# Kernel tuning notes

Hardware: AMD Instinct MI355X
Metric: run time of the kernel (lower is better)

Reference implementation:

```python
import jax, jax.numpy as jnp
import numpy as np

CHUNK = 64  # chunk size for chunkwise delta-rule


def l2norm(x, eps=1e-6):
    return x * jax.lax.rsqrt(jnp.sum(x * x, axis=-1, keepdims=True) + eps)


def delta_rule_chunked(q, k, v, beta):
    """Chunkwise-parallel DeltaNet delta rule.

    Recurrence (per head): S_t = S_{t-1} + k_t u_t^T with
      u_t = beta_t * (v_t - S_{t-1}^T k_t),   o_t = S_t^T q_t.
    q,k,v: [B,H,L,D]; beta: [B,H,L]. Returns o: [B,H,L,D].
    """
    B, H, L, D = q.shape
    n = L // CHUNK
    def to_chunks(t):
        return jnp.moveaxis(t.reshape(B, H, n, CHUNK, *t.shape[4:] if t.ndim > 4 else ()) if False else t.reshape(B, H, n, CHUNK, -1) if t.ndim == 4 else t.reshape(B, H, n, CHUNK), 2, 0)
    qc = jnp.moveaxis(q.reshape(B, H, n, CHUNK, D), 2, 0)  # [n,B,H,C,D]
    kc = jnp.moveaxis(k.reshape(B, H, n, CHUNK, D), 2, 0)
    vc = jnp.moveaxis(v.reshape(B, H, n, CHUNK, D), 2, 0)
    bc = jnp.moveaxis(beta.reshape(B, H, n, CHUNK), 2, 0)   # [n,B,H,C]
    strict = jnp.tril(jnp.ones((CHUNK, CHUNK), bool), -1)
    incl = jnp.tril(jnp.ones((CHUNK, CHUNK), bool))
    eye = jnp.eye(CHUNK, dtype=q.dtype)

    def step(S, inp):
        qi, ki, vi, bi = inp  # [B,H,C,D], [B,H,C]
        kk = jnp.einsum('bhid,bhjd->bhij', ki, ki)            # [B,H,C,C]
        # Unit lower-triangular system (I + B*strict_tril(K K^T)) U = B*(V - K S)
        T = eye + jnp.where(strict, bi[..., :, None] * kk, 0.0)
        rhs = bi[..., None] * (vi - jnp.einsum('bhcd,bhde->bhce', ki, S))
        U = jax.scipy.linalg.solve_triangular(T, rhs, lower=True)
        qk = jnp.einsum('bhid,bhjd->bhij', qi, ki)
        O = jnp.einsum('bhcd,bhde->bhce', qi, S) \
            + jnp.einsum('bhij,bhje->bhie', jnp.where(incl, qk, 0.0), U)
        S_new = S + jnp.einsum('bhcd,bhce->bhde', ki, U)      # [B,H,D,D]
        return S_new, O

    S0 = jnp.zeros((B, H, D, D), q.dtype)
    _, O = jax.lax.scan(step, S0, (qc, kc, vc, bc))
    return jnp.moveaxis(O, 0, 2).reshape(B, H, L, D)


def setup_inputs() -> dict:
    key = jax.random.key(0)
    ks = jax.random.split(key, 7)
    B, C, Hh, Ww = 8, 768, 64, 64
    n_heads = 12
    s = 1.0 / np.sqrt(C)
    x = jax.random.normal(ks[0], (B, C, Hh, Ww), jnp.float32)
    Wq = jax.random.normal(ks[1], (C, C), jnp.float32) * s
    Wk = jax.random.normal(ks[2], (C, C), jnp.float32) * s
    Wv = jax.random.normal(ks[3], (C, C), jnp.float32) * s
    Wb = jax.random.normal(ks[4], (C, n_heads), jnp.float32) * s
    Wo = jax.random.normal(ks[5], (C, C), jnp.float32) * s
    return {"x": x, "Wq": Wq, "Wk": Wk, "Wv": Wv, "Wb": Wb, "Wo": Wo}


def reference(x, Wq, Wk, Wv, Wb, Wo):
    B, C, Hh, Ww = x.shape
    L = Hh * Ww
    n_heads = Wb.shape[1]
    D = C // n_heads
    t = x.reshape(B, C, L).transpose(0, 2, 1)                 # [B,L,C] tokens
    def heads(z):
        return z.reshape(B, L, n_heads, D).transpose(0, 2, 1, 3)  # [B,H,L,D]
    q = l2norm(heads(jax.nn.silu(t @ Wq)))
    k = l2norm(heads(jax.nn.silu(t @ Wk)))
    v = heads(jax.nn.silu(t @ Wv))
    beta = jax.nn.sigmoid(t @ Wb).transpose(0, 2, 1)          # [B,H,L]
    o = delta_rule_chunked(q, k, v, beta)                     # [B,H,L,D]
    o = o.transpose(0, 2, 1, 3).reshape(B, L, C)
    y = o @ Wo
    out = t + y                                               # residual
    return out.transpose(0, 2, 1).reshape(B, C, Hh, Ww)
```

## Files before the change

kernel.cpp:

```cpp
#include <hip/hip_runtime.h>


#define B_  8
#define C_  768
#define L_  4096
#define NH_ 12
#define D_  64
#define NC_ 64
#define BH_ 96

typedef unsigned short ushort_t;
typedef float f32x4 __attribute__((ext_vector_type(4)));
typedef unsigned short u16x4 __attribute__((ext_vector_type(4)));
typedef unsigned short u16x8 __attribute__((ext_vector_type(8)));
using short8 = __attribute__((ext_vector_type(8))) short;

__device__ __forceinline__ float b2f(ushort_t u) {
  union { unsigned u; float f; } x; x.u = ((unsigned)u) << 16; return x.f;
}
__device__ __forceinline__ ushort_t f2b(float f) {
  union { float f; unsigned u; } x; x.f = f;
  unsigned r = (x.u + 0x7FFFu + ((x.u >> 16) & 1u)) >> 16;
  return (ushort_t)r;
}
__device__ __forceinline__ f32x4 mfma16(short8 a, short8 b, f32x4 c) {
  return __builtin_amdgcn_mfma_f32_16x16x32_bf16(a, b, c, 0, 0, 0);
}
__device__ __forceinline__ void gload16(const ushort_t* g, ushort_t* l) {
  __builtin_amdgcn_global_load_lds(
      (const __attribute__((address_space(1))) void*)(g),
      (__attribute__((address_space(3))) void*)(l), 16, 0, 0);
}

#define SWZ(e, i) (((e) * 64) + ((i) ^ (((e) & 7) << 3)))

__global__ __launch_bounds__(256) void k_wprep(
    const float* __restrict__ W, ushort_t* __restrict__ hi,
    ushort_t* __restrict__ lo) {
  __shared__ float ts[64 * 65];
  int tid = threadIdx.x;
  int c0 = blockIdx.x * 64;
  int n0 = blockIdx.y * 64;
  #pragma unroll
  for (int it = 0; it < 4; ++it) {
    int e = tid + it * 256;
    int r = e >> 4, c4 = (e & 15) * 4;
    *(f32x4*)&ts[r * 65 + c4] =
        *(const f32x4*)(W + (size_t)(c0 + r) * C_ + n0 + c4);
  }
  __syncthreads();
  #pragma unroll
  for (int it = 0; it < 4; ++it) {
    int e = tid + it * 256;
    int n = e >> 4, r4 = (e & 15) * 4;
    u16x4 hv, lv;
    #pragma unroll
    for (int q = 0; q < 4; ++q) {
      float w = ts[(r4 + q) * 65 + n];
      ushort_t h = f2b(w);
      hv[q] = h;
      lv[q] = f2b(w - b2f(h));
    }
    *(u16x4*)(hi + (size_t)(n0 + n) * C_ + c0 + r4) = hv;
    *(u16x4*)(lo + (size_t)(n0 + n) * C_ + c0 + r4) = lv;
  }
}

__global__ __launch_bounds__(256) void k_xtr(
    const float* __restrict__ x, ushort_t* __restrict__ hi,
    ushort_t* __restrict__ lo) {
  __shared__ float ts[64 * 65];
  int tid = threadIdx.x;
  int l0 = blockIdx.x * 64;
  int c0 = blockIdx.y * 64;
  int b = blockIdx.z;
  const float* xb = x + (size_t)b * C_ * L_;
  #pragma unroll
  for (int it = 0; it < 4; ++it) {
    int e = tid + it * 256;
    int ci = e >> 4, l4 = (e & 15) * 4;
    *(f32x4*)&ts[ci * 65 + l4] =
        *(const f32x4*)(xb + (size_t)(c0 + ci) * L_ + l0 + l4);
  }
  __syncthreads();
  #pragma unroll
  for (int it = 0; it < 4; ++it) {
    int e = tid + it * 256;
    int li = e >> 4, c4 = (e & 15) * 4;
    u16x4 hv, lv;
    #pragma unroll
    for (int q = 0; q < 4; ++q) {
      float w = ts[(c4 + q) * 65 + li];
      ushort_t h = f2b(w);
      hv[q] = h;
      lv[q] = f2b(w - b2f(h));
    }
    size_t base = ((size_t)b * L_ + l0 + li) * C_ + c0 + c4;
    *(u16x4*)(hi + base) = hv;
    *(u16x4*)(lo + base) = lv;
  }
}

__global__ __launch_bounds__(256) void k_beta(
    const float* __restrict__ x, const float* __restrict__ Wb,
    float* __restrict__ beta) {
  __shared__ float wb[C_ * NH_];
  int tid = threadIdx.x;
  for (int i = tid; i < C_ * NH_; i += 256) wb[i] = Wb[i];
  __syncthreads();
  int b = blockIdx.y;
  int l = blockIdx.x * 256 + tid;
  f32x4 a0 = {0.f, 0.f, 0.f, 0.f}, a1 = a0, a2 = a0;
  const float* xb = x + (size_t)b * C_ * L_ + l;
  for (int c = 0; c < C_; ++c) {
    float xv = xb[(size_t)c * L_];
    const f32x4* wr = (const f32x4*)&wb[c * NH_];
    a0 += xv * wr[0]; a1 += xv * wr[1]; a2 += xv * wr[2];
  }
  float* bp = beta + (size_t)b * NH_ * L_ + l;
  #pragma unroll
  for (int h = 0; h < 4; ++h) {
    bp[(size_t)h * L_]       = 1.f / (1.f + expf(-a0[h]));
    bp[(size_t)(h + 4) * L_] = 1.f / (1.f + expf(-a1[h]));
    bp[(size_t)(h + 8) * L_] = 1.f / (1.f + expf(-a2[h]));
  }
}

__global__ __launch_bounds__(256) void k_qkv(
    const ushort_t* __restrict__ xhi, const ushort_t* __restrict__ xlo,
    const ushort_t* __restrict__ whi, const ushort_t* __restrict__ wlo,
    ushort_t* __restrict__ qout, ushort_t* __restrict__ kout,
    ushort_t* __restrict__ vout) {
  __shared__ __align__(16) ushort_t Ah[128 * 32];
  __shared__ __align__(16) ushort_t Al[128 * 32];
  __shared__ __align__(16) ushort_t Bh[128 * 32];
  __shared__ __align__(16) ushort_t Bl[128 * 32];
  int tid = threadIdx.x;
  int row0 = blockIdx.x * 128;
  int n0   = blockIdx.y * 128;
  int wid = tid >> 6, lane = tid & 63;
  int lr = lane & 15, lk = lane >> 4;
  f32x4 acc[2][8];
  #pragma unroll
  for (int mf = 0; mf < 2; ++mf)
    #pragma unroll
    for (int nf = 0; nf < 8; ++nf) acc[mf][nf] = (f32x4){0.f, 0.f, 0.f, 0.f};
  const ushort_t* ga  = xhi + (size_t)row0 * C_;
  const ushort_t* gal = xlo + (size_t)row0 * C_;
  const ushort_t* gb  = whi + (size_t)n0 * C_;
  const ushort_t* gbl = wlo + (size_t)n0 * C_;
  int ra0 = wid * 32 + lr, ra1 = wid * 32 + 16 + lr;
  int ua0 = ra0 * 4 + (lk ^ ((ra0 >> 1) & 3));
  int ua1 = ra1 * 4 + (lk ^ ((ra1 >> 1) & 3));
  for (int kb = 0; kb < C_; kb += 32) {
    if (kb) __syncthreads();
    #pragma unroll
    for (int c = 0; c < 2; ++c) {
      int u = tid + c * 256;
      int r = u >> 2, sp = u & 3;
      int s = sp ^ ((r >> 1) & 3);
      size_t goff = (size_t)r * C_ + kb + s * 8;
      gload16(ga  + goff, &Ah[u * 8]);
      gload16(gal + goff, &Al[u * 8]);
      gload16(gb  + goff, &Bh[u * 8]);
      gload16(gbl + goff, &Bl[u * 8]);
    }
    __syncthreads();
    short8 ah0 = *(const short8*)&Ah[ua0 * 8];
    short8 al0 = *(const short8*)&Al[ua0 * 8];
    short8 ah1 = *(const short8*)&Ah[ua1 * 8];
    short8 al1 = *(const short8*)&Al[ua1 * 8];
    #pragma unroll
    for (int nf = 0; nf < 8; ++nf) {
      int rb = nf * 16 + lr;
      int ub = rb * 4 + (lk ^ ((rb >> 1) & 3));
      short8 bh = *(const short8*)&Bh[ub * 8];
      short8 bl = *(const short8*)&Bl[ub * 8];
      acc[0][nf] = mfma16(ah0, bh, acc[0][nf]);
      acc[0][nf] = mfma16(al0, bh, acc[0][nf]);
      acc[0][nf] = mfma16(ah0, bl, acc[0][nf]);
      acc[1][nf] = mfma16(ah1, bh, acc[1][nf]);
      acc[1][nf] = mfma16(al1, bh, acc[1][nf]);
      acc[1][nf] = mfma16(ah1, bl, acc[1][nf]);
    }
  }
  #pragma unroll
  for (int mf = 0; mf < 2; ++mf)
    #pragma unroll
    for (int nf = 0; nf < 8; ++nf)
      #pragma unroll
      for (int rr = 0; rr < 4; ++rr) {
        float xv = acc[mf][nf][rr];
        acc[mf][nf][rr] = xv / (1.f + expf(-xv));
      }
  int proj = n0 / 768;
  if (proj < 2) {
    #pragma unroll
    for (int mf = 0; mf < 2; ++mf)
      #pragma unroll
      for (int rr = 0; rr < 4; ++rr)
        #pragma unroll
        for (int g = 0; g < 2; ++g) {
          float ss = 0.f;
          #pragma unroll
          for (int nf = 4 * g; nf < 4 * g + 4; ++nf)
            ss += acc[mf][nf][rr] * acc[mf][nf][rr];
          ss += __shfl_xor(ss, 1); ss += __shfl_xor(ss, 2);
          ss += __shfl_xor(ss, 4); ss += __shfl_xor(ss, 8);
          float rs = rsqrtf(ss + 1e-6f);
          #pragma unroll
          for (int nf = 4 * g; nf < 4 * g + 4; ++nf) acc[mf][nf][rr] *= rs;
        }
  }
  ushort_t* outp = (proj == 0) ? qout : ((proj == 1) ? kout : vout);
  int nc0 = n0 - proj * 768;
  #pragma unroll
  for (int mf = 0; mf < 2; ++mf) {
    int row = row0 + wid * 32 + mf * 16 + lk * 4;
    int b = row >> 12, l = row & 4095;
    #pragma unroll
    for (int nf = 0; nf < 8; ++nf) {
      int ncol = nc0 + nf * 16 + lr;
      int h = ncol >> 6, d = ncol & 63;
      ushort_t* op = outp + (((size_t)b * NH_ + h) * L_ + l) * 64 + d;
      #pragma unroll
      for (int rr = 0; rr < 4; ++rr)
        op[(size_t)rr * 64] = f2b(acc[mf][nf][rr]);
    }
  }
}

__global__ __launch_bounds__(256) void k_pre2(
    const ushort_t* __restrict__ qg, ushort_t* kg, ushort_t* vg,
    const float* __restrict__ betag, ushort_t* __restrict__ kwg,
    ushort_t* __restrict__ aqg) {
  __shared__ float As[64 * 68];
  __shared__ float XK[64 * 68];
  __shared__ float XV[64 * 68];
  int tid = threadIdx.x;
  int nc = blockIdx.x, bh = blockIdx.y;
  const size_t cb = ((size_t)bh * 64 + nc) * 4096;
  const float* bb = betag + (size_t)bh * L_ + nc * 64;
  int wid = tid >> 6, lane = tid & 63;
  int lr = lane & 15, lk = lane >> 4;
  short8 kbf[4][2], ka[2], qa[2];
  #pragma unroll
  for (int nf = 0; nf < 4; ++nf)
    #pragma unroll
    for (int ks = 0; ks < 2; ++ks)
      kbf[nf][ks] = *(const short8*)(kg + cb +
          (size_t)(nf * 16 + lr) * 64 + ks * 32 + lk * 8);
  #pragma unroll
  for (int ks = 0; ks < 2; ++ks) {
    ka[ks] = *(const short8*)(kg + cb + (size_t)(wid * 16 + lr) * 64 + ks * 32 + lk * 8);
    qa[ks] = *(const short8*)(qg + cb + (size_t)(wid * 16 + lr) * 64 + ks * 32 + lk * 8);
  }
  f32x4 kk[4], qk[4];
  #pragma unroll
  for (int nf = 0; nf < 4; ++nf) {
    kk[nf] = (f32x4){0.f, 0.f, 0.f, 0.f};
    qk[nf] = (f32x4){0.f, 0.f, 0.f, 0.f};
    kk[nf] = mfma16(ka[0], kbf[nf][0], kk[nf]);
    kk[nf] = mfma16(ka[1], kbf[nf][1], kk[nf]);
    qk[nf] = mfma16(qa[0], kbf[nf][0], qk[nf]);
    qk[nf] = mfma16(qa[1], kbf[nf][1], qk[nf]);
  }
  float bi[4];
  #pragma unroll
  for (int r = 0; r < 4; ++r) bi[r] = bb[wid * 16 + lk * 4 + r];
  #pragma unroll
  for (int r = 0; r < 4; ++r) {
    int i = wid * 16 + lk * 4 + r;
    #pragma unroll
    for (int nf = 0; nf < 4; ++nf) {
      int j = nf * 16 + lr;
      As[i * 68 + j] = (j < i) ? bi[r] * kk[nf][r] : 0.f;
      aqg[cb + (size_t)i * 64 + j] = (j <= i) ? f2b(qk[nf][r]) : (ushort_t)0;
    }
  }
  #pragma unroll
  for (int it = 0; it < 2; ++it) {
    int e = tid + it * 256;
    int i = e >> 3, c0 = (e & 7) * 8;
    float bv = bb[i];
    u16x8 kv8 = *(const u16x8*)(kg + cb + (size_t)i * 64 + c0);
    u16x8 vv8 = *(const u16x8*)(vg + cb + (size_t)i * 64 + c0);
    f32x4 klo = {bv*b2f(kv8[0]), bv*b2f(kv8[1]), bv*b2f(kv8[2]), bv*b2f(kv8[3])};
    f32x4 khi = {bv*b2f(kv8[4]), bv*b2f(kv8[5]), bv*b2f(kv8[6]), bv*b2f(kv8[7])};
    f32x4 vlo = {bv*b2f(vv8[0]), bv*b2f(vv8[1]), bv*b2f(vv8[2]), bv*b2f(vv8[3])};
    f32x4 vhi = {bv*b2f(vv8[4]), bv*b2f(vv8[5]), bv*b2f(vv8[6]), bv*b2f(vv8[7])};
    *(f32x4*)&XK[i * 68 + c0]     = klo;
    *(f32x4*)&XK[i * 68 + c0 + 4] = khi;
    *(f32x4*)&XV[i * 68 + c0]     = vlo;
    *(f32x4*)&XV[i * 68 + c0 + 4] = vhi;
  }
  __syncthreads();
  if (tid < 128) {
    float* Xc = (tid < 64) ? (XK + tid) : (XV + (tid - 64));
    float xr[32];
    #pragma unroll
    for (int i = 0; i < 32; ++i) xr[i] = Xc[i * 68];
    #pragma unroll
    for (int i = 1; i < 32; ++i) {
      float xi = xr[i];
      #pragma unroll
      for (int jb = 0; jb <= (i >> 2); ++jb) {
        f32x4 a4 = *(const f32x4*)&As[i * 68 + jb * 4];
        xi -= a4[0]*xr[jb*4] + a4[1]*xr[jb*4+1] + a4[2]*xr[jb*4+2] + a4[3]*xr[jb*4+3];
      }
      xr[i] = xi;
    }
    #pragma unroll
    for (int i = 1; i < 32; ++i) Xc[i * 68] = xr[i];
  } else {
    int ks = wid - 2;
    #pragma unroll
    for (int nf = 0; nf < 4; ++nf)
      #pragma unroll
      for (int jj = 0; jj < 8; ++jj) {
        int d = ks * 32 + lk * 8 + jj;
        kg[cb + (size_t)d * 64 + nf * 16 + lr] = (ushort_t)kbf[nf][ks][jj];
      }
  }
  __syncthreads();
  if (tid >= 128) {
    int col = tid - 128;
    float* Xc = (col < 64) ? (XK + col) : (XV + (col - 64));
    float xr[32];
    #pragma unroll
    for (int i = 0; i < 32; ++i) xr[i] = Xc[(32 + i) * 68];
    #pragma unroll
    for (int jb = 0; jb < 8; ++jb) {
      float xt0 = Xc[(jb*4+0)*68], xt1 = Xc[(jb*4+1)*68];
      float xt2 = Xc[(jb*4+2)*68], xt3 = Xc[(jb*4+3)*68];
      #pragma unroll
      for (int i = 0; i < 32; ++i) {
        f32x4 a4 = *(const f32x4*)&As[(32 + i) * 68 + jb * 4];
        xr[i] -= a4[0]*xt0 + a4[1]*xt1 + a4[2]*xt2 + a4[3]*xt3;
      }
    }
    #pragma unroll
    for (int i = 1; i < 32; ++i) {
      float xi = xr[i];
      #pragma unroll
      for (int jb = 8; jb <= ((32 + i) >> 2); ++jb) {
        f32x4 a4 = *(const f32x4*)&As[(32 + i) * 68 + jb * 4];
        xi -= a4[0]*xr[jb*4-32] + a4[1]*xr[jb*4-31]
            + a4[2]*xr[jb*4-30] + a4[3]*xr[jb*4-29];
      }
      xr[i] = xi;
    }
    #pragma unroll
    for (int i = 0; i < 32; ++i) Xc[(32 + i) * 68] = xr[i];
  } else {
    #pragma unroll
    for (int it = 0; it < 4; ++it) {
      int u = tid + it * 128;
      int i = u >> 4, d0 = (u & 15) * 4;
      f32x4 v4 = *(const f32x4*)&XK[i * 68 + d0];
      u16x4 pk = {f2b(v4[0]), f2b(v4[1]), f2b(v4[2]), f2b(v4[3])};
      *(u16x4*)(kwg + cb + (size_t)i * 64 + d0) = pk;
      f32x4 w4 = *(const f32x4*)&XV[i * 68 + d0];
      u16x4 pv = {f2b(w4[0]), f2b(w4[1]), f2b(w4[2]), f2b(w4[3])};
      *(u16x4*)(vg + cb + (size_t)i * 64 + d0) = pv;
    }
  }
  __syncthreads();
  #pragma unroll
  for (int it = 0; it < 2; ++it) {
    int u = tid + it * 256;
    int i = 32 + (u >> 4), d0 = (u & 15) * 4;
    f32x4 v4 = *(const f32x4*)&XK[i * 68 + d0];
    u16x4 pk = {f2b(v4[0]), f2b(v4[1]), f2b(v4[2]), f2b(v4[3])};
    *(u16x4*)(kwg + cb + (size_t)i * 64 + d0) = pk;
    f32x4 w4 = *(const f32x4*)&XV[i * 68 + d0];
    u16x4 pv = {f2b(w4[0]), f2b(w4[1]), f2b(w4[2]), f2b(w4[3])};
    *(u16x4*)(vg + cb + (size_t)i * 64 + d0) = pv;
  }
}

__global__ __launch_bounds__(256) void k_seq(
    const ushort_t* __restrict__ qg,  const ushort_t* __restrict__ ktg,
    const ushort_t* __restrict__ kwg, const ushort_t* __restrict__ vwg,
    const ushort_t* __restrict__ aqg, ushort_t* __restrict__ og) {
  __shared__ float    STs[64 * 64];
  __shared__ ushort_t SbT[64 * 64];
  __shared__ ushort_t UT [64 * 64];
  int tid = threadIdx.x, bh = blockIdx.x;
  int w  = tid >> 6, l = tid & 63;
  int lr = l & 15, lk = l >> 4;
  int mrow = w * 16 + lr;
  int r0   = w * 16 + lk * 4;
  for (int i = tid; i < 4096; i += 256) { STs[i] = 0.f; SbT[i] = 0; }
  int b = bh / NH_, h = bh % NH_;
  ushort_t* ob = og + (size_t)b * L_ * C_ + h * 64;
  __syncthreads();
  for (int nc = 0; nc < NC_; ++nc) {
    const size_t cb = ((size_t)bh * 64 + nc) * 4096;
    const ushort_t* Kw = kwg + cb;
    const ushort_t* Qc = qg  + cb;
    const ushort_t* Aq = aqg + cb;
    const ushort_t* KT = ktg + cb;
    const ushort_t* Vw = vwg + cb;
    short8 a_kw0 = *(const short8*)(Kw + mrow * 64 + lk * 8);
    short8 a_kw1 = *(const short8*)(Kw + mrow * 64 + 32 + lk * 8);
    short8 a_q0  = *(const short8*)(Qc + mrow * 64 + lk * 8);
    short8 a_q1  = *(const short8*)(Qc + mrow * 64 + 32 + lk * 8);
    short8 a_aq0 = *(const short8*)(Aq + mrow * 64 + lk * 8);
    short8 a_aq1 = *(const short8*)(Aq + mrow * 64 + 32 + lk * 8);
    short8 a_kt0 = *(const short8*)(KT + mrow * 64 + lk * 8);
    short8 a_kt1 = *(const short8*)(KT + mrow * 64 + 32 + lk * 8);
    float vwv[4][4];
    #pragma unroll
    for (int t = 0; t < 4; ++t)
      #pragma unroll
      for (int r = 0; r < 4; ++r)
        vwv[t][r] = b2f(Vw[(size_t)(r0 + r) * 64 + t * 16 + lr]);
    #pragma unroll
    for (int t = 0; t < 4; ++t) {
      int e = t * 16 + lr;
      f32x4 acc = {0.f, 0.f, 0.f, 0.f};
      short8 b0 = *(const short8*)(SbT + SWZ(e, lk * 8));
      short8 b1 = *(const short8*)(SbT + SWZ(e, 32 + lk * 8));
      acc = mfma16(a_kw0, b0, acc);
      acc = mfma16(a_kw1, b1, acc);
      u16x4 uo;
      #pragma unroll
      for (int r = 0; r < 4; ++r) uo[r] = f2b(vwv[t][r] - acc[r]);
      *(u16x4*)(UT + SWZ(e, r0)) = uo;
    }
    __syncthreads();
    #pragma unroll
    for (int t = 0; t < 4; ++t) {
      int e = t * 16 + lr;
      f32x4 acc = {0.f, 0.f, 0.f, 0.f};
      short8 s0 = *(const short8*)(SbT + SWZ(e, lk * 8));
      short8 s1 = *(const short8*)(SbT + SWZ(e, 32 + lk * 8));
      short8 u0 = *(const short8*)(UT  + SWZ(e, lk * 8));
      short8 u1 = *(const short8*)(UT  + SWZ(e, 32 + lk * 8));
      acc = mfma16(a_q0,  s0, acc);
      acc = mfma16(a_q1,  s1, acc);
      acc = mfma16(a_aq0, u0, acc);
      acc = mfma16(a_aq1, u1, acc);
      #pragma unroll
      for (int r = 0; r < 4; ++r)
        ob[(size_t)(nc * 64 + r0 + r) * C_ + e] = f2b(acc[r]);
    }
    __syncthreads();
    #pragma unroll
    for (int t = 0; t < 4; ++t) {
      int e = t * 16 + lr;
      f32x4 acc = {0.f, 0.f, 0.f, 0.f};
      short8 u0 = *(const short8*)(UT + SWZ(e, lk * 8));
      short8 u1 = *(const short8*)(UT + SWZ(e, 32 + lk * 8));
      acc = mfma16(a_kt0, u0, acc);
      acc = mfma16(a_kt1, u1, acc);
      float* sp = &STs[SWZ(e, r0)];
      f32x4 sv = *(const f32x4*)sp;
      sv += acc;
      *(f32x4*)sp = sv;
      u16x4 sb = {f2b(sv[0]), f2b(sv[1]), f2b(sv[2]), f2b(sv[3])};
      *(u16x4*)(SbT + SWZ(e, r0)) = sb;
    }
    __syncthreads();
  }
}

__global__ __launch_bounds__(256) void k_final2(
    const ushort_t* __restrict__ o, const ushort_t* __restrict__ wot,
    const float* __restrict__ x, float* __restrict__ outp) {
  __shared__ __align__(16) ushort_t Ats[128 * 32];
  __shared__ __align__(16) ushort_t Bts[128 * 32];
  int tid = threadIdx.x;
  int b = blockIdx.z;
  int c0 = blockIdx.y * 128;
  int l0 = blockIdx.x * 128;
  int wid = tid >> 6, lane = tid & 63;
  int lr = lane & 15, lk = lane >> 4;
  f32x4 acc[2][8];
  #pragma unroll
  for (int mf = 0; mf < 2; ++mf)
    #pragma unroll
    for (int nf = 0; nf < 8; ++nf) acc[mf][nf] = (f32x4){0.f, 0.f, 0.f, 0.f};
  const ushort_t* ga = wot + (size_t)c0 * C_;
  const ushort_t* gb = o + ((size_t)b * L_ + l0) * C_;
  int ra0 = wid * 32 + lr, ra1 = wid * 32 + 16 + lr;
  int ua0 = ra0 * 4 + (lk ^ ((ra0 >> 1) & 3));
  int ua1 = ra1 * 4 + (lk ^ ((ra1 >> 1) & 3));
  for (int kb = 0; kb < C_; kb += 32) {
    if (kb) __syncthreads();
    #pragma unroll
    for (int c = 0; c < 2; ++c) {
      int u = tid + c * 256;
      int r = u >> 2, sp = u & 3;
      int s = sp ^ ((r >> 1) & 3);
      size_t goff = (size_t)r * C_ + kb + s * 8;
      gload16(ga + goff, &Ats[u * 8]);
      gload16(gb + goff, &Bts[u * 8]);
    }
    __syncthreads();
    short8 a0 = *(const short8*)&Ats[ua0 * 8];
    short8 a1 = *(const short8*)&Ats[ua1 * 8];
    #pragma unroll
    for (int nf = 0; nf < 8; ++nf) {
      int rb = nf * 16 + lr;
      int ub = rb * 4 + (lk ^ ((rb >> 1) & 3));
      short8 bv = *(const short8*)&Bts[ub * 8];
      acc[0][nf] = mfma16(a0, bv, acc[0][nf]);
      acc[1][nf] = mfma16(a1, bv, acc[1][nf]);
    }
  }
  #pragma unroll
  for (int mf = 0; mf < 2; ++mf) {
    int cc0 = c0 + wid * 32 + mf * 16 + lk * 4;
    #pragma unroll
    for (int nf = 0; nf < 8; ++nf) {
      int ll = l0 + nf * 16 + lr;
      #pragma unroll
      for (int rr = 0; rr < 4; ++rr) {
        size_t idx = ((size_t)b * C_ + cc0 + rr) * L_ + ll;
        outp[idx] = acc[mf][nf][rr] + x[idx];
      }
    }
  }
}

extern "C" void kernel_launch(void* const* d_in, const int* in_sizes, int n_in,
                              void* d_out, int out_size, void* d_ws, size_t ws_size,
                              hipStream_t stream) {
  (void)in_sizes; (void)n_in; (void)out_size; (void)ws_size;
  const float* x  = (const float*)d_in[0];
  const float* Wq = (const float*)d_in[1];
  const float* Wk = (const float*)d_in[2];
  const float* Wv = (const float*)d_in[3];
  const float* Wb = (const float*)d_in[4];
  const float* Wo = (const float*)d_in[5];
  float* outp = (float*)d_out;

  const size_t NE = (size_t)B_ * NH_ * L_ * D_;
  const size_t WE = (size_t)C_ * C_;
  ushort_t* q    = (ushort_t*)d_ws;
  ushort_t* kbuf = q + NE;
  ushort_t* v    = kbuf + NE;
  float*    beta = (float*)(v + NE);
  ushort_t* o    = (ushort_t*)(beta + (size_t)B_ * NH_ * L_);
  ushort_t* kw   = o + NE;
  ushort_t* aqk  = kw + NE;
  ushort_t* wt   = aqk + NE;
  ushort_t* xt_hi = aqk;
  ushort_t* xt_lo = kw;
  ushort_t* wt_q = wt, *wt_o = wt + 3 * WE;
  ushort_t* wl_q = o;

  k_wprep<<<dim3(12, 12), 256, 0, stream>>>(Wq, wt_q, wl_q);
  k_wprep<<<dim3(12, 12), 256, 0, stream>>>(Wk, wt + WE, o + WE);
  k_wprep<<<dim3(12, 12), 256, 0, stream>>>(Wv, wt + 2 * WE, o + 2 * WE);
  k_wprep<<<dim3(12, 12), 256, 0, stream>>>(Wo, wt_o, o + 3 * WE);
  k_xtr<<<dim3(L_ / 64, C_ / 64, B_), 256, 0, stream>>>(x, xt_hi, xt_lo);
  k_beta<<<dim3(L_ / 256, B_), 256, 0, stream>>>(x, Wb, beta);
  k_qkv<<<dim3((B_ * L_) / 128, 18), 256, 0, stream>>>(
      xt_hi, xt_lo, wt_q, wl_q, q, kbuf, v);
  k_pre2<<<dim3(NC_, BH_), 256, 0, stream>>>(q, kbuf, v, beta, kw, aqk);
  k_seq<<<dim3(BH_), 256, 0, stream>>>(q, kbuf, kw, v, aqk, o);
  k_final2<<<dim3(L_ / 128, C_ / 128, B_), 256, 0, stream>>>(o, wt_o, x, outp);
}
```

Baseline: 1.078 ms.

## Rewrite QKV GEMM with 256x256 tiles, double-buffered LDS and split-bf16 segments

The QKV projection GEMM now uses 512-thread blocks computing 256x256 tiles with a 64-wide K step and double-buffered LDS. Global loads for the next stage are interleaved with MFMA work, with explicit barriers, waitcnts and setprio. Block indices are swizzled for L2 locality. The three hi/lo bf16 product terms are restructured into three sequential K sweeps (hi*hi, lo*hi, hi*lo) over one accumulator instead of three MFMAs per fragment. This is meant to raise arithmetic intensity and overlap memory with compute, at the cost of heavy register and LDS use (128 KB of LDS) and a fragile hand-scheduled sync pattern.

```diff
diff --git a/kernel.cpp b/kernel.cpp
--- a/kernel.cpp
+++ b/kernel.cpp
@@ -126,106 +126,144 @@
   }
 }
 
-__global__ __launch_bounds__(256) void k_qkv(
+__global__ __launch_bounds__(512, 2) void k_qkv8(
     const ushort_t* __restrict__ xhi, const ushort_t* __restrict__ xlo,
     const ushort_t* __restrict__ whi, const ushort_t* __restrict__ wlo,
     ushort_t* __restrict__ qout, ushort_t* __restrict__ kout,
     ushort_t* __restrict__ vout) {
-  __shared__ __align__(16) ushort_t Ah[128 * 32];
-  __shared__ __align__(16) ushort_t Al[128 * 32];
-  __shared__ __align__(16) ushort_t Bh[128 * 32];
-  __shared__ __align__(16) ushort_t Bl[128 * 32];
+  __shared__ __align__(16) ushort_t LA[2][256 * 64];
+  __shared__ __align__(16) ushort_t LB[2][256 * 64];
   int tid = threadIdx.x;
-  int row0 = blockIdx.x * 128;
-  int n0   = blockIdx.y * 128;
+  int bid = blockIdx.x;
+  int swz = (bid & 7) * 144 + (bid >> 3);
+  int bx = swz & 127, by = swz >> 7;
+  int row0 = bx * 256, n0 = by * 256;
   int wid = tid >> 6, lane = tid & 63;
+  int wm = wid >> 2, wn = wid & 3;
   int lr = lane & 15, lk = lane >> 4;
-  f32x4 acc[2][8];
-  #pragma unroll
-  for (int mf = 0; mf < 2; ++mf)
-    #pragma unroll
-    for (int nf = 0; nf < 8; ++nf) acc[mf][nf] = (f32x4){0.f, 0.f, 0.f, 0.f};
-  const ushort_t* ga  = xhi + (size_t)row0 * C_;
-  const ushort_t* gal = xlo + (size_t)row0 * C_;
-  const ushort_t* gb  = whi + (size_t)n0 * C_;
-  const ushort_t* gbl = wlo + (size_t)n0 * C_;
-  int ra0 = wid * 32 + lr, ra1 = wid * 32 + 16 + lr;
-  int ua0 = ra0 * 4 + (lk ^ ((ra0 >> 1) & 3));
-  int ua1 = ra1 * 4 + (lk ^ ((ra1 >> 1) & 3));
-  for (int kb = 0; kb < C_; kb += 32) {
-    if (kb) __syncthreads();
-    #pragma unroll
-    for (int c = 0; c < 2; ++c) {
-      int u = tid + c * 256;
-      int r = u >> 2, sp = u & 3;
-      int s = sp ^ ((r >> 1) & 3);
-      size_t goff = (size_t)r * C_ + kb + s * 8;
-      gload16(ga  + goff, &Ah[u * 8]);
-      gload16(gal + goff, &Al[u * 8]);
-      gload16(gb  + goff, &Bh[u * 8]);
-      gload16(gbl + goff, &Bl[u * 8]);
-    }
-    __syncthreads();
-    short8 ah0 = *(const short8*)&Ah[ua0 * 8];
-    short8 al0 = *(const short8*)&Al[ua0 * 8];
-    short8 ah1 = *(const short8*)&Ah[ua1 * 8];
-    short8 al1 = *(const short8*)&Al[ua1 * 8];
-    #pragma unroll
-    for (int nf = 0; nf < 8; ++nf) {
-      int rb = nf * 16 + lr;
-      int ub = rb * 4 + (lk ^ ((rb >> 1) & 3));
-      short8 bh = *(const short8*)&Bh[ub * 8];
-      short8 bl = *(const short8*)&Bl[ub * 8];
-      acc[0][nf] = mfma16(ah0, bh, acc[0][nf]);
-      acc[0][nf] = mfma16(al0, bh, acc[0][nf]);
-      acc[0][nf] = mfma16(ah0, bl, acc[0][nf]);
-      acc[1][nf] = mfma16(ah1, bh, acc[1][nf]);
-      acc[1][nf] = mfma16(al1, bh, acc[1][nf]);
-      acc[1][nf] = mfma16(ah1, bl, acc[1][nf]);
-    }
-  }
-  #pragma unroll
-  for (int mf = 0; mf < 2; ++mf)
-    #pragma unroll
-    for (int nf = 0; nf < 8; ++nf)
+  int m7 = lr & 7;
+  int aofs[4], bofs[4];
+  #pragma unroll
+  for (int j = 0; j < 4; ++j) {
+    int u = tid + j * 512;
+    int r = u >> 3, s = (u & 7) ^ (r & 7);
+    aofs[j] = (row0 + r) * C_ + s * 8;
+    bofs[j] = (n0 + r) * C_ + s * 8;
+  }
+  f32x4 acc[8][4];
+  #pragma unroll
+  for (int mf = 0; mf < 8; ++mf)
+    #pragma unroll
+    for (int nf = 0; nf < 4; ++nf) acc[mf][nf] = (f32x4){0.f, 0.f, 0.f, 0.f};
+  #pragma unroll
+  for (int j = 0; j < 4; ++j) {
+    gload16(xhi + aofs[j], &LA[0][(tid + j * 512) * 8]);
+    gload16(whi + bofs[j], &LB[0][(tid + j * 512) * 8]);
+  }
+  __syncthreads();
+  #pragma unroll 1
+  for (int t = 0; t < 36; ++t) {
+    int bb = t & 1, nb = bb ^ 1;
+    int tt = t + 1;
+    bool st = (tt < 36);
+    int seg = tt / 12;
+    int kseg = (tt - seg * 12) * 64;
+    const ushort_t* Asrc = (seg == 1) ? xlo : xhi;
+    const ushort_t* Bsrc = (seg == 2) ? wlo : whi;
+    short8 bF[4][2];
+    #pragma unroll
+    for (int q = 0; q < 4; ++q) {
+      short8 aF[2][2];
+      int ra0 = wm * 128 + q * 32 + lr;
+      int ra1 = ra0 + 16;
+      #pragma unroll
+      for (int ks = 0; ks < 2; ++ks) {
+        int g = ks * 4 + lk;
+        aF[0][ks] = *(const short8*)&LA[bb][(ra0 * 8 + (g ^ m7)) * 8];
+        aF[1][ks] = *(const short8*)&LA[bb][(ra1 * 8 + (g ^ m7)) * 8];
+      }
+      if (q == 0) {
+        #pragma unroll
+        for (int nf = 0; nf < 4; ++nf) {
+          int rb = wn * 64 + nf * 16 + lr;
+          #pragma unroll
+          for (int ks = 0; ks < 2; ++ks) {
+            int g = ks * 4 + lk;
+            bF[nf][ks] = *(const short8*)&LB[bb][(rb * 8 + (g ^ m7)) * 8];
+          }
+        }
+      }
+      if (st) {
+        if (q == 0) {
+          gload16(Asrc + kseg + aofs[0], &LA[nb][(tid) * 8]);
+          gload16(Asrc + kseg + aofs[1], &LA[nb][(tid + 512) * 8]);
+          gload16(Asrc + kseg + aofs[2], &LA[nb][(tid + 1024) * 8]);
+          gload16(Asrc + kseg + aofs[3], &LA[nb][(tid + 1536) * 8]);
+        }
+        if (q == 1) {
+          gload16(Bsrc + kseg + bofs[0], &LB[nb][(tid) * 8]);
+          gload16(Bsrc + kseg + bofs[1], &LB[nb][(tid + 512) * 8]);
+        }
+        if (q == 2) {
+          gload16(Bsrc + kseg + bofs[2], &LB[nb][(tid + 1024) * 8]);
+          gload16(Bsrc + kseg + bofs[3], &LB[nb][(tid + 1536) * 8]);
+        }
+      }
+      __builtin_amdgcn_s_barrier();
+      asm volatile("s_waitcnt lgkmcnt(0)" ::: "memory");
+      __builtin_amdgcn_sched_barrier(0);
+      __builtin_amdgcn_s_setprio(1);
+      #pragma unroll
+      for (int nf = 0; nf < 4; ++nf) {
+        acc[2 * q][nf]     = mfma16(aF[0][0], bF[nf][0], acc[2 * q][nf]);
+        acc[2 * q][nf]     = mfma16(aF[0][1], bF[nf][1], acc[2 * q][nf]);
+        acc[2 * q + 1][nf] = mfma16(aF[1][0], bF[nf][0], acc[2 * q + 1][nf]);
+        acc[2 * q + 1][nf] = mfma16(aF[1][1], bF[nf][1], acc[2 * q + 1][nf]);
+      }
+      __builtin_amdgcn_s_setprio(0);
+      if (q == 3) asm volatile("s_waitcnt vmcnt(0)" ::: "memory");
+      __builtin_amdgcn_s_barrier();
+    }
+  }
+  #pragma unroll
+  for (int mf = 0; mf < 8; ++mf)
+    #pragma unroll
+    for (int nf = 0; nf < 4; ++nf)
       #pragma unroll
       for (int rr = 0; rr < 4; ++rr) {
         float xv = acc[mf][nf][rr];
         acc[mf][nf][rr] = xv / (1.f + expf(-xv));
       }
-  int proj = n0 / 768;
+  int colbase = n0 + wn * 64;
+  int proj = colbase / 768;
   if (proj < 2) {
     #pragma unroll
-    for (int mf = 0; mf < 2; ++mf)
+    for (int mf = 0; mf < 8; ++mf)
+      #pragma unroll
+      for (int rr = 0; rr < 4; ++rr) {
+        float ss = 0.f;
+        #pragma unroll
+        for (int nf = 0; nf < 4; ++nf) ss += acc[mf][nf][rr] * acc[mf][nf][rr];
+        ss += __shfl_xor(ss, 1); ss += __shfl_xor(ss, 2);
+        ss += __shfl_xor(ss, 4); ss += __shfl_xor(ss, 8);
+        float rs = rsqrtf(ss + 1e-6f);
+        #pragma unroll
+        for (int nf = 0; nf < 4; ++nf) acc[mf][nf][rr] *= rs;
+      }
+  }
+  ushort_t* outsel = (proj == 0) ? qout : ((proj == 1) ? kout : vout);
+  int h = (colbase - proj * 768) >> 6;
+  #pragma unroll
+  for (int mf = 0; mf < 8; ++mf) {
+    int row = row0 + wm * 128 + mf * 16 + lk * 4;
+    int b = row >> 12, l = row & 4095;
+    ushort_t* op0 = outsel + (((size_t)b * NH_ + h) * L_ + l) * 64;
+    #pragma unroll
+    for (int nf = 0; nf < 4; ++nf) {
+      int d = nf * 16 + lr;
       #pragma unroll
       for (int rr = 0; rr < 4; ++rr)
-        #pragma unroll
-        for (int g = 0; g < 2; ++g) {
-          float ss = 0.f;
-          #pragma unroll
-          for (int nf = 4 * g; nf < 4 * g + 4; ++nf)
-            ss += acc[mf][nf][rr] * acc[mf][nf][rr];
-          ss += __shfl_xor(ss, 1); ss += __shfl_xor(ss, 2);
-          ss += __shfl_xor(ss, 4); ss += __shfl_xor(ss, 8);
-          float rs = rsqrtf(ss + 1e-6f);
-          #pragma unroll
-          for (int nf = 4 * g; nf < 4 * g + 4; ++nf) acc[mf][nf][rr] *= rs;
-        }
-  }
-  ushort_t* outp = (proj == 0) ? qout : ((proj == 1) ? kout : vout);
-  int nc0 = n0 - proj * 768;
-  #pragma unroll
-  for (int mf = 0; mf < 2; ++mf) {
-    int row = row0 + wid * 32 + mf * 16 + lk * 4;
-    int b = row >> 12, l = row & 4095;
-    #pragma unroll
-    for (int nf = 0; nf < 8; ++nf) {
-      int ncol = nc0 + nf * 16 + lr;
-      int h = ncol >> 6, d = ncol & 63;
-      ushort_t* op = outp + (((size_t)b * NH_ + h) * L_ + l) * 64 + d;
-      #pragma unroll
-      for (int rr = 0; rr < 4; ++rr)
-        op[(size_t)rr * 64] = f2b(acc[mf][nf][rr]);
+        op0[(size_t)rr * 64 + d] = f2b(acc[mf][nf][rr]);
     }
   }
 }
@@ -558,7 +596,7 @@
   k_wprep<<<dim3(12, 12), 256, 0, stream>>>(Wo, wt_o, o + 3 * WE);
   k_xtr<<<dim3(L_ / 64, C_ / 64, B_), 256, 0, stream>>>(x, xt_hi, xt_lo);
   k_beta<<<dim3(L_ / 256, B_), 256, 0, stream>>>(x, Wb, beta);
-  k_qkv<<<dim3((B_ * L_) / 128, 18), 256, 0, stream>>>(
+  k_qkv8<<<dim3((B_ * L_ / 256) * (2304 / 256)), 512, 0, stream>>>(
       xt_hi, xt_lo, wt_q, wl_q, q, kbuf, v);
   k_pre2<<<dim3(NC_, BH_), 256, 0, stream>>>(q, kbuf, v, beta, kw, aqk);
   k_seq<<<dim3(BH_), 256, 0, stream>>>(q, kbuf, kw, v, aqk, o);
```

Result: no change. 1.099 ms (+1.9%).
